# Optimization experiments

Hardware: AMD Instinct MI355X
Metric: run time of the kernel (lower is better)

## Reference

```python
import jax, jax.numpy as jnp
import numpy as np

B, S, HID = 2, 2048, 1024
NH = 16
DK = HID // NH


def setup_inputs() -> dict:
    key0 = jax.random.key(0)
    ks = jax.random.split(key0, 16)
    inp = {
        "query": jax.random.normal(ks[0], (B, S, HID), dtype=jnp.float32),
        "key": jax.random.normal(ks[1], (B, S, HID), dtype=jnp.float32),
        "value": jax.random.normal(ks[2], (B, S, HID), dtype=jnp.float32),
        "bias": jax.random.uniform(ks[3], (B, S), dtype=jnp.float32),
        "mask": jax.random.randint(ks[4], (B, 1, S), 0, 2, dtype=jnp.int32),
        "wq": jax.random.normal(ks[5], (HID, HID), dtype=jnp.float32) * 0.02,
        "bq": jax.random.normal(ks[6], (HID,), dtype=jnp.float32) * 0.02,
        "wk": jax.random.normal(ks[7], (HID, HID), dtype=jnp.float32) * 0.02,
        "bk": jax.random.normal(ks[8], (HID,), dtype=jnp.float32) * 0.02,
        "wv": jax.random.normal(ks[9], (HID, HID), dtype=jnp.float32) * 0.02,
        "bv": jax.random.normal(ks[10], (HID,), dtype=jnp.float32) * 0.02,
        "wo": jax.random.normal(ks[11], (HID, HID), dtype=jnp.float32) * 0.02,
        "bo": jax.random.normal(ks[12], (HID,), dtype=jnp.float32) * 0.02,
    }
    return inp


def reference(query, key, value, bias, mask, wq, bq, wk, bk, wv, bv, wo, bo):
    b, s, hid = query.shape
    # attn_bias_type == 'both': gate K and V with per-token scalar bias
    # (dropout is eval-mode identity): x + p[..., None] * x
    key = key + bias[:, :, None] * key
    value = value + bias[:, :, None] * value

    def proj(x, w, bb):
        # torch Linear: x @ W.T + b, then split heads -> [b, nh, s, dk]
        y = x @ w.T + bb
        return y.reshape(b, s, NH, DK).transpose(0, 2, 1, 3)

    q = proj(query, wq, bq)
    k = proj(key, wk, bk)
    v = proj(value, wv, bv)

    scores = jnp.einsum("bhqd,bhkd->bhqk", q, k) / jnp.sqrt(jnp.asarray(DK, q.dtype))
    m = mask[:, None]  # [b,1,1,s] broadcast over heads and query positions
    scores = jnp.where(m == 0, jnp.asarray(-10000.0, scores.dtype), scores)
    p_attn = jax.nn.softmax(scores, axis=-1)
    x = jnp.einsum("bhqk,bhkd->bhqd", p_attn, v)
    x = x.transpose(0, 2, 1, 3).reshape(b, s, hid)
    return x @ wo.T + bo
```

## Files before the change

### kernel.cpp

```cpp
#include <hip/hip_runtime.h>
#include <stdint.h>

#define NB   2
#define SS   2048
#define HIDN 1024
#define NHEAD 16
#define DKK  64

typedef __attribute__((ext_vector_type(8))) short bf16x8;
typedef __attribute__((ext_vector_type(4))) float f32x4;

__device__ __forceinline__ uint16_t f2bf(float f) {
    uint32_t u = __float_as_uint(f);
    u += 0x7FFF + ((u >> 16) & 1);
    return (uint16_t)(u >> 16);
}
__device__ __forceinline__ uint32_t pk2(float f0, float f1) {
    uint32_t u0 = __float_as_uint(f0);
    uint32_t u1 = __float_as_uint(f1);
    u0 += 0x7FFF + ((u0 >> 16) & 1);
    u1 += 0x7FFF + ((u1 >> 16) & 1);
    return (u0 >> 16) | (u1 & 0xFFFF0000u);
}
__device__ __forceinline__ uint32_t cvtpk(float lo, float hi) {
    uint32_t r;
    asm("v_cvt_pk_bf16_f32 %0, %1, %2" : "=v"(r) : "v"(lo), "v"(hi));
    return r;
}
__device__ __forceinline__ float exp2_fast(float x) {
    float r;
    asm("v_exp_f32 %0, %1" : "=v"(r) : "v"(x));
    return r;
}
__device__ __forceinline__ uint4 pack8(const float* __restrict__ s, float sc) {
    float4 a = *(const float4*)s;
    float4 b = *(const float4*)(s + 4);
    uint4 r;
    r.x = pk2(sc * a.x, sc * a.y);
    r.y = pk2(sc * a.z, sc * a.w);
    r.z = pk2(sc * b.x, sc * b.y);
    r.w = pk2(sc * b.z, sc * b.w);
    return r;
}
__device__ __forceinline__ void gl_lds16(const uint16_t* g, uint16_t* l) {
    __builtin_amdgcn_global_load_lds((const __attribute__((address_space(1))) void*)g,
                                     (__attribute__((address_space(3))) void*)l,
                                     16, 0, 0);
}

__global__ __launch_bounds__(256, 4)
void cvt_all(const float* __restrict__ q, const float* __restrict__ k,
             const float* __restrict__ v, const float* __restrict__ bias,
             const float* __restrict__ w0, const float* __restrict__ w1,
             const float* __restrict__ w2, const float* __restrict__ w3,
             uint16_t* __restrict__ q16, uint16_t* __restrict__ k16,
             uint16_t* __restrict__ v16, uint16_t* __restrict__ w16o)
{
    int i = blockIdx.x * 256 + threadIdx.x;
    if (i < 524288) {
        size_t e = (size_t)i * 8;
        float sc = 1.0f + bias[i >> 7];
        *(uint4*)(q16 + e) = pack8(q + e, 1.0f);
        *(uint4*)(k16 + e) = pack8(k + e, sc);
        *(uint4*)(v16 + e) = pack8(v + e, sc);
    } else {
        int j = i - 524288;
        const float* src = (j < 131072) ? w0 : (j < 262144) ? w1
                         : (j < 393216) ? w2 : w3;
        size_t e = (size_t)(j & 131071) * 8;
        *(uint4*)(w16o + (size_t)(j >> 17) * 1048576 + e) = pack8(src + e, 1.0f);
    }
}

__device__ __forceinline__ void gemm_core(const uint16_t* __restrict__ A,
                                          const uint16_t* __restrict__ W,
                                          uint16_t* __restrict__ As0,
                                          uint16_t* __restrict__ As1,
                                          uint16_t* __restrict__ Bs0,
                                          uint16_t* __restrict__ Bs1,
                                          int m0, int n0,
                                          f32x4 acc[4][2])
{
    const int t    = threadIdx.x;
    const int w    = t >> 6;
    const int lane = t & 63;
    const int q    = lane >> 4;
    const int lr   = lane & 15;
    const int wr   = (w >> 1) * 64;
    const int wc   = (w & 1) * 32;
    const int srow = lane >> 3;
    const int sg   = (lane & 7) ^ srow;

#pragma unroll
    for (int c = 0; c < 4; ++c) {
        int r = w * 32 + c * 8;
        gl_lds16(A + (size_t)(m0 + r + srow) * HIDN + sg * 8, As0 + r * 64);
    }
#pragma unroll
    for (int c = 0; c < 2; ++c) {
        int r = w * 16 + c * 8;
        gl_lds16(W + (size_t)(n0 + r + srow) * HIDN + sg * 8, Bs0 + r * 64);
    }

    for (int it = 0; it < 16; ++it) {
        uint16_t* Asc = (it & 1) ? As1 : As0;
        uint16_t* Bsc = (it & 1) ? Bs1 : Bs0;
        uint16_t* Asn = (it & 1) ? As0 : As1;
        uint16_t* Bsn = (it & 1) ? Bs0 : Bs1;
        __syncthreads();
        if (it + 1 < 16) {
            int k0 = (it + 1) * 64;
#pragma unroll
            for (int c = 0; c < 4; ++c) {
                int r = w * 32 + c * 8;
                gl_lds16(A + (size_t)(m0 + r + srow) * HIDN + k0 + sg * 8,
                         Asn + r * 64);
            }
#pragma unroll
            for (int c = 0; c < 2; ++c) {
                int r = w * 16 + c * 8;
                gl_lds16(W + (size_t)(n0 + r + srow) * HIDN + k0 + sg * 8,
                         Bsn + r * 64);
            }
        }
        bf16x8 af[2][4], bfr[2][2];
#pragma unroll
        for (int s = 0; s < 2; ++s) {
#pragma unroll
            for (int i = 0; i < 4; ++i)
                af[s][i] = *(const bf16x8*)&Asc[(wr + i * 16 + lr) * 64 +
                                                (((s * 4 + q) ^ (lr & 7)) * 8)];
#pragma unroll
            for (int j = 0; j < 2; ++j)
                bfr[s][j] = *(const bf16x8*)&Bsc[(wc + j * 16 + lr) * 64 +
                                                 (((s * 4 + q) ^ (lr & 7)) * 8)];
        }
#pragma unroll
        for (int s = 0; s < 2; ++s)
#pragma unroll
            for (int i = 0; i < 4; ++i)
#pragma unroll
                for (int j = 0; j < 2; ++j)
                    acc[i][j] = __builtin_amdgcn_mfma_f32_16x16x32_bf16(
                        af[s][i], bfr[s][j], acc[i][j], 0, 0, 0);
    }
}

__global__ __launch_bounds__(256, 3)
void gemm_qkv(const uint16_t* __restrict__ Qin, const uint16_t* __restrict__ Kin,
              const uint16_t* __restrict__ Vin, const uint16_t* __restrict__ W16,
              const float* __restrict__ bq, const float* __restrict__ bk,
              const float* __restrict__ bv,
              uint16_t* __restrict__ Qb, uint16_t* __restrict__ Kb,
              uint16_t* __restrict__ Vtb)
{
    __shared__ __align__(16) uint16_t As[2][128 * 64];
    __shared__ __align__(16) uint16_t Bs[2][64 * 64];

    const int z = blockIdx.z;
    const uint16_t* A    = (z == 0) ? Qin : (z == 1) ? Kin : Vin;
    const uint16_t* W    = W16 + (size_t)z * 1048576;
    const float*    bias = (z == 0) ? bq : (z == 1) ? bk : bv;
    const float     osc  = (z == 0) ? 0.125f * 1.44269504f : 1.0f;

    const int t    = threadIdx.x;
    const int w    = t >> 6;
    const int lane = t & 63;
    const int q    = lane >> 4;
    const int lr   = lane & 15;
    const int wr   = (w >> 1) * 64;
    const int wc   = (w & 1) * 32;
    const int m0   = blockIdx.y * 128;
    const int n0   = blockIdx.x * 64;

    f32x4 acc[4][2] = {};
    gemm_core(A, W, As[0], As[1], Bs[0], Bs[1], m0, n0, acc);

    if (z < 2) {
        uint16_t* o = (z == 0) ? Qb : Kb;
#pragma unroll
        for (int i = 0; i < 4; ++i)
#pragma unroll
            for (int j = 0; j < 2; ++j) {
                int gn = n0 + wc + j * 16 + lr;
                float bvx = bias[gn];
#pragma unroll
                for (int r = 0; r < 4; ++r) {
                    int row = m0 + wr + i * 16 + q * 4 + r;
                    int b = row >> 11, s = row & 2047;
                    size_t dst = (size_t)b * (NHEAD * SS * DKK)
                               + (size_t)(gn >> 6) * (SS * DKK)
                               + (size_t)s * DKK + (gn & 63);
                    o[dst] = f2bf((acc[i][j][r] + bvx) * osc);
                }
            }
    } else {
        __syncthreads();
        uint16_t* Tr = (uint16_t*)As;
#pragma unroll
        for (int i = 0; i < 4; ++i)
#pragma unroll
            for (int j = 0; j < 2; ++j) {
                int d = wc + j * 16 + lr;
                float bvx = bias[n0 + d];
#pragma unroll
                for (int r = 0; r < 4; ++r) {
                    int sl = wr + i * 16 + q * 4 + r;
                    Tr[d * 136 + sl] = f2bf(acc[i][j][r] + bvx);
                }
            }
        __syncthreads();
        int b = m0 >> 11, h = n0 >> 6;
#pragma unroll
        for (int p = 0; p < 4; ++p) {
            int idx = p * 256 + t;
            int d   = idx >> 4;
            int sc8 = (idx & 15) * 8;
            size_t dst = ((size_t)(b * NHEAD + h) * DKK + d) * SS
                       + (m0 & 2047) + sc8;
            *(uint4*)&Vtb[dst] = *(const uint4*)&Tr[d * 136 + sc8];
        }
    }
}

__global__ __launch_bounds__(256, 3)
void gemm_out(const uint16_t* __restrict__ Xb, const uint16_t* __restrict__ W,
              const float* __restrict__ bias, float* __restrict__ out)
{
    __shared__ __align__(16) uint16_t As[2][128 * 64];
    __shared__ __align__(16) uint16_t Bs[2][64 * 64];

    const int t    = threadIdx.x;
    const int w    = t >> 6;
    const int lane = t & 63;
    const int q    = lane >> 4;
    const int lr   = lane & 15;
    const int wr   = (w >> 1) * 64;
    const int wc   = (w & 1) * 32;
    const int m0   = blockIdx.y * 128;
    const int n0   = blockIdx.x * 64;

    f32x4 acc[4][2] = {};
    gemm_core(Xb, W, As[0], As[1], Bs[0], Bs[1], m0, n0, acc);

#pragma unroll
    for (int i = 0; i < 4; ++i)
#pragma unroll
        for (int j = 0; j < 2; ++j) {
            int gn = n0 + wc + j * 16 + lr;
            float bvx = bias[gn];
#pragma unroll
            for (int r = 0; r < 4; ++r) {
                int row = m0 + wr + i * 16 + q * 4 + r;
                out[(size_t)row * HIDN + gn] = acc[i][j][r] + bvx;
            }
        }
}

__global__ __launch_bounds__(512, 4)
void flash_attn(const uint16_t* __restrict__ Qg, const uint16_t* __restrict__ Kg,
                const uint16_t* __restrict__ Vtg, const int* __restrict__ mask,
                uint16_t* __restrict__ X)
{
    __shared__ __align__(16) uint16_t QP[128 * 72];
    __shared__ __align__(16) uint16_t Ks[64 * 72];
    __shared__ __align__(16) uint16_t Vs[64 * 72];
    __shared__ __align__(16) float Amf[SS];

    const int t    = threadIdx.x;
    const int w    = t >> 6;
    const int lane = t & 63;
    const int q    = lane >> 4;
    const int lr   = lane & 15;
    const int bh   = blockIdx.y;
    const int b    = bh >> 4;
    const int h    = bh & 15;
    const int q0   = blockIdx.x * 128;
    const size_t head = (size_t)bh * SS * DKK;

#pragma unroll
    for (int p = 0; p < 2; ++p) {
        int idx = p * 512 + t;
        int row = idx >> 3;
        int col = (idx & 7) * 8;
        *(uint4*)&QP[row * 72 + col] =
            *(const uint4*)(Qg + head + (size_t)(q0 + row) * DKK + col);
    }
#pragma unroll
    for (int p = 0; p < 4; ++p) {
        int i = p * 512 + t;
        Amf[i] = (mask[b * SS + i] == 0) ? -14426.95f : 0.0f;
    }

    const int srow = t >> 3;
    const int scol = (t & 7) * 8;
    uint4 kreg = *(const uint4*)(Kg + head + (size_t)srow * DKK + scol);
    uint4 vreg = *(const uint4*)(Vtg + head + (size_t)srow * SS + scol);

    __syncthreads();

    bf16x8 qf[2];
#pragma unroll
    for (int s = 0; s < 2; ++s)
        qf[s] = *(const bf16x8*)&QP[(w * 16 + lr) * 72 + s * 32 + q * 8];

    float mst = -1e30f, lst = 0.0f;
    f32x4 oacc[4] = {};

    for (int kv0 = 0; kv0 < SS; kv0 += 64) {
        *(uint4*)&Ks[srow * 72 + scol] = kreg;
        *(uint4*)&Vs[srow * 72 + scol] = vreg;
        __syncthreads();

        if (kv0 + 64 < SS) {
            kreg = *(const uint4*)(Kg + head + (size_t)(kv0 + 64 + srow) * DKK + scol);
            vreg = *(const uint4*)(Vtg + head + (size_t)srow * SS + kv0 + 64 + scol);
        }

        f32x4 st[4];
#pragma unroll
        for (int ni = 0; ni < 4; ++ni) {
            bf16x8 kf0 = *(const bf16x8*)&Ks[(ni * 16 + lr) * 72 + 0  + q * 8];
            bf16x8 kf1 = *(const bf16x8*)&Ks[(ni * 16 + lr) * 72 + 32 + q * 8];
            f32x4 z = {0.0f, 0.0f, 0.0f, 0.0f};
            z = __builtin_amdgcn_mfma_f32_16x16x32_bf16(kf0, qf[0], z, 0, 0, 0);
            z = __builtin_amdgcn_mfma_f32_16x16x32_bf16(kf1, qf[1], z, 0, 0, 0);
            st[ni] = z;
        }

        float rmax = -1e30f;
#pragma unroll
        for (int ni = 0; ni < 4; ++ni) {
            float4 am = *(const float4*)&Amf[kv0 + ni * 16 + q * 4];
            st[ni][0] += am.x; st[ni][1] += am.y;
            st[ni][2] += am.z; st[ni][3] += am.w;
#pragma unroll
            for (int r = 0; r < 4; ++r) rmax = fmaxf(rmax, st[ni][r]);
        }
        rmax = fmaxf(rmax, __shfl_xor(rmax, 16));
        rmax = fmaxf(rmax, __shfl_xor(rmax, 32));

        if (__any(rmax > mst + 11.5f)) {
            float mnew  = fmaxf(mst, rmax);
            float alpha = exp2_fast(mst - mnew);
            mst = mnew;
            lst *= alpha;
#pragma unroll
            for (int dj = 0; dj < 4; ++dj) {
                oacc[dj][0] *= alpha; oacc[dj][1] *= alpha;
                oacc[dj][2] *= alpha; oacc[dj][3] *= alpha;
            }
        }

        float rsum = 0.0f;
#pragma unroll
        for (int ni = 0; ni < 4; ++ni) {
            float p0 = exp2_fast(st[ni][0] - mst);
            float p1 = exp2_fast(st[ni][1] - mst);
            float p2 = exp2_fast(st[ni][2] - mst);
            float p3 = exp2_fast(st[ni][3] - mst);
            rsum += (p0 + p1) + (p2 + p3);
            uint2 pw = make_uint2(cvtpk(p0, p1), cvtpk(p2, p3));
            *(uint2*)&QP[(w * 16 + lr) * 72 + ni * 16 + q * 4] = pw;
        }
        rsum += __shfl_xor(rsum, 16);
        rsum += __shfl_xor(rsum, 32);
        lst += rsum;

#pragma unroll
        for (int ks = 0; ks < 2; ++ks) {
            bf16x8 pfB = *(const bf16x8*)&QP[(w * 16 + lr) * 72 + ks * 32 + q * 8];
#pragma unroll
            for (int dj = 0; dj < 4; ++dj) {
                bf16x8 vfA = *(const bf16x8*)&Vs[(dj * 16 + lr) * 72 + ks * 32 + q * 8];
                oacc[dj] = __builtin_amdgcn_mfma_f32_16x16x32_bf16(vfA, pfB, oacc[dj], 0, 0, 0);
            }
        }
        __syncthreads();
    }

    {
        float inv = 1.0f / lst;
        int s = q0 + w * 16 + lr;
        uint16_t* xp = X + (size_t)(b * SS + s) * HIDN + h * DKK;
#pragma unroll
        for (int dj = 0; dj < 4; ++dj) {
            uint2 pw = make_uint2(cvtpk(oacc[dj][0] * inv, oacc[dj][1] * inv),
                                  cvtpk(oacc[dj][2] * inv, oacc[dj][3] * inv));
            *(uint2*)(xp + dj * 16 + q * 4) = pw;
        }
    }
}

extern "C" void kernel_launch(void* const* d_in, const int* in_sizes, int n_in,
                              void* d_out, int out_size, void* d_ws, size_t ws_size,
                              hipStream_t stream) {
    const float* query = (const float*)d_in[0];
    const float* key   = (const float*)d_in[1];
    const float* value = (const float*)d_in[2];
    const float* bias  = (const float*)d_in[3];
    const int*   mask  = (const int*)d_in[4];
    const float* wq = (const float*)d_in[5];
    const float* bq = (const float*)d_in[6];
    const float* wk = (const float*)d_in[7];
    const float* bk = (const float*)d_in[8];
    const float* wv = (const float*)d_in[9];
    const float* bv = (const float*)d_in[10];
    const float* wo = (const float*)d_in[11];
    const float* bo = (const float*)d_in[12];

    const size_t TEN = (size_t)NB * SS * HIDN;
    uint16_t* Qin = (uint16_t*)d_ws;
    uint16_t* Kin = Qin + TEN;
    uint16_t* Vin = Kin + TEN;
    uint16_t* W16 = Vin + TEN;
    uint16_t* Qb  = W16 + 4 * 1048576;
    uint16_t* Kb  = Qb + TEN;
    uint16_t* Vtb = Kb + TEN;
    uint16_t* Xb  = Qin;

    cvt_all<<<4096, 256, 0, stream>>>(query, key, value, bias,
                                      wq, wk, wv, wo, Qin, Kin, Vin, W16);
    gemm_qkv<<<dim3(16, 32, 3), 256, 0, stream>>>(Qin, Kin, Vin, W16,
                                                  bq, bk, bv, Qb, Kb, Vtb);
    flash_attn<<<dim3(SS / 128, NB * NHEAD), 512, 0, stream>>>(Qb, Kb, Vtb, mask, Xb);
    gemm_out<<<dim3(16, 32), 256, 0, stream>>>(Xb, W16 + 3 * 1048576, bo, (float*)d_out);
}
```

Measured before the change: 250.2 us.

## Shrink flash-attention blocks to 64 queries with 4 waves and MFMA priority hints

Halves the query tile per block from 128 to 64 rows and runs 4 waves instead of 8, which doubles the grid so more blocks can spread across CUs. Q fragments are now loaded straight from global memory into registers instead of going through shared memory, and the P buffer shrinks to match. Each thread stages two K/V chunks per step. s_setprio raises wave priority around the MFMA sections. The cost is that every K/V tile is loaded and mask-expanded twice as often across the whole grid.

```diff
diff --git a/kernel.cpp b/kernel.cpp
--- a/kernel.cpp
+++ b/kernel.cpp
@@ -257,12 +257,12 @@
         }
 }
 
-__global__ __launch_bounds__(512, 4)
+__global__ __launch_bounds__(256, 4)
 void flash_attn(const uint16_t* __restrict__ Qg, const uint16_t* __restrict__ Kg,
                 const uint16_t* __restrict__ Vtg, const int* __restrict__ mask,
                 uint16_t* __restrict__ X)
 {
-    __shared__ __align__(16) uint16_t QP[128 * 72];
+    __shared__ __align__(16) uint16_t Ps[64 * 72];
     __shared__ __align__(16) uint16_t Ks[64 * 72];
     __shared__ __align__(16) uint16_t Vs[64 * 72];
     __shared__ __align__(16) float Amf[SS];
@@ -275,49 +275,58 @@
     const int bh   = blockIdx.y;
     const int b    = bh >> 4;
     const int h    = bh & 15;
-    const int q0   = blockIdx.x * 128;
+    const int q0   = blockIdx.x * 64;
     const size_t head = (size_t)bh * SS * DKK;
 
-#pragma unroll
-    for (int p = 0; p < 2; ++p) {
-        int idx = p * 512 + t;
-        int row = idx >> 3;
-        int col = (idx & 7) * 8;
-        *(uint4*)&QP[row * 72 + col] =
-            *(const uint4*)(Qg + head + (size_t)(q0 + row) * DKK + col);
-    }
-#pragma unroll
-    for (int p = 0; p < 4; ++p) {
-        int i = p * 512 + t;
+    bf16x8 qf[2];
+#pragma unroll
+    for (int s = 0; s < 2; ++s)
+        qf[s] = *(const bf16x8*)(Qg + head + (size_t)(q0 + w * 16 + lr) * DKK
+                                 + s * 32 + q * 8);
+
+    uint4 kreg[2], vreg[2];
+#pragma unroll
+    for (int c = 0; c < 2; ++c) {
+        int g = c * 256 + t;
+        int row = g >> 3, col = (g & 7) * 8;
+        kreg[c] = *(const uint4*)(Kg + head + (size_t)row * DKK + col);
+        vreg[c] = *(const uint4*)(Vtg + head + (size_t)row * SS + col);
+    }
+
+#pragma unroll
+    for (int p = 0; p < 8; ++p) {
+        int i = p * 256 + t;
         Amf[i] = (mask[b * SS + i] == 0) ? -14426.95f : 0.0f;
     }
-
-    const int srow = t >> 3;
-    const int scol = (t & 7) * 8;
-    uint4 kreg = *(const uint4*)(Kg + head + (size_t)srow * DKK + scol);
-    uint4 vreg = *(const uint4*)(Vtg + head + (size_t)srow * SS + scol);
-
     __syncthreads();
-
-    bf16x8 qf[2];
-#pragma unroll
-    for (int s = 0; s < 2; ++s)
-        qf[s] = *(const bf16x8*)&QP[(w * 16 + lr) * 72 + s * 32 + q * 8];
 
     float mst = -1e30f, lst = 0.0f;
     f32x4 oacc[4] = {};
 
     for (int kv0 = 0; kv0 < SS; kv0 += 64) {
-        *(uint4*)&Ks[srow * 72 + scol] = kreg;
-        *(uint4*)&Vs[srow * 72 + scol] = vreg;
+#pragma unroll
+        for (int c = 0; c < 2; ++c) {
+            int g = c * 256 + t;
+            int row = g >> 3, col = (g & 7) * 8;
+            *(uint4*)&Ks[row * 72 + col] = kreg[c];
+            *(uint4*)&Vs[row * 72 + col] = vreg[c];
+        }
         __syncthreads();
 
         if (kv0 + 64 < SS) {
-            kreg = *(const uint4*)(Kg + head + (size_t)(kv0 + 64 + srow) * DKK + scol);
-            vreg = *(const uint4*)(Vtg + head + (size_t)srow * SS + kv0 + 64 + scol);
+#pragma unroll
+            for (int c = 0; c < 2; ++c) {
+                int g = c * 256 + t;
+                int row = g >> 3, col = (g & 7) * 8;
+                kreg[c] = *(const uint4*)(Kg + head +
+                          (size_t)(kv0 + 64 + row) * DKK + col);
+                vreg[c] = *(const uint4*)(Vtg + head +
+                          (size_t)row * SS + kv0 + 64 + col);
+            }
         }
 
         f32x4 st[4];
+        __builtin_amdgcn_s_setprio(1);
 #pragma unroll
         for (int ni = 0; ni < 4; ++ni) {
             bf16x8 kf0 = *(const bf16x8*)&Ks[(ni * 16 + lr) * 72 + 0  + q * 8];
@@ -327,6 +336,7 @@
             z = __builtin_amdgcn_mfma_f32_16x16x32_bf16(kf1, qf[1], z, 0, 0, 0);
             st[ni] = z;
         }
+        __builtin_amdgcn_s_setprio(0);
 
         float rmax = -1e30f;
 #pragma unroll
@@ -361,21 +371,23 @@
             float p3 = exp2_fast(st[ni][3] - mst);
             rsum += (p0 + p1) + (p2 + p3);
             uint2 pw = make_uint2(cvtpk(p0, p1), cvtpk(p2, p3));
-            *(uint2*)&QP[(w * 16 + lr) * 72 + ni * 16 + q * 4] = pw;
+            *(uint2*)&Ps[(w * 16 + lr) * 72 + ni * 16 + q * 4] = pw;
         }
         rsum += __shfl_xor(rsum, 16);
         rsum += __shfl_xor(rsum, 32);
         lst += rsum;
 
+        __builtin_amdgcn_s_setprio(1);
 #pragma unroll
         for (int ks = 0; ks < 2; ++ks) {
-            bf16x8 pfB = *(const bf16x8*)&QP[(w * 16 + lr) * 72 + ks * 32 + q * 8];
+            bf16x8 pfB = *(const bf16x8*)&Ps[(w * 16 + lr) * 72 + ks * 32 + q * 8];
 #pragma unroll
             for (int dj = 0; dj < 4; ++dj) {
                 bf16x8 vfA = *(const bf16x8*)&Vs[(dj * 16 + lr) * 72 + ks * 32 + q * 8];
                 oacc[dj] = __builtin_amdgcn_mfma_f32_16x16x32_bf16(vfA, pfB, oacc[dj], 0, 0, 0);
             }
         }
+        __builtin_amdgcn_s_setprio(0);
         __syncthreads();
     }
 
@@ -423,6 +435,6 @@
                                       wq, wk, wv, wo, Qin, Kin, Vin, W16);
     gemm_qkv<<<dim3(16, 32, 3), 256, 0, stream>>>(Qin, Kin, Vin, W16,
                                                   bq, bk, bv, Qb, Kb, Vtb);
-    flash_attn<<<dim3(SS / 128, NB * NHEAD), 512, 0, stream>>>(Qb, Kb, Vtb, mask, Xb);
+    flash_attn<<<dim3(SS / 64, NB * NHEAD), 256, 0, stream>>>(Qb, Kb, Vtb, mask, Xb);
     gemm_out<<<dim3(16, 32), 256, 0, stream>>>(Xb, W16 + 3 * 1048576, bo, (float*)d_out);
 }
```

Measured after the change: 323.1 us. +29.1%, slower.

## Enlarge GEMM tiles to 128x128 and drop LDS double buffering

Applied to the files above, without the earlier changes.

The QKV and output projection GEMMs move from 128x64 to 128x128 block tiles, with each wave computing a 64x64 sub-tile, which halves the grid and doubles operand reuse per LDS load. The LDS double buffer is replaced by a single buffer that loads, syncs, computes and syncs again, so global loads no longer overlap MFMA work within a block. The V-transpose epilogue now writes two heads per block through LDS in two passes. This trades latency hiding and occupancy (more accumulator registers, fewer blocks) for less redundant global and LDS traffic.

```diff
diff --git a/kernel.cpp b/kernel.cpp
--- a/kernel.cpp
+++ b/kernel.cpp
@@ -74,12 +74,10 @@
 
 __device__ __forceinline__ void gemm_core(const uint16_t* __restrict__ A,
                                           const uint16_t* __restrict__ W,
-                                          uint16_t* __restrict__ As0,
-                                          uint16_t* __restrict__ As1,
-                                          uint16_t* __restrict__ Bs0,
-                                          uint16_t* __restrict__ Bs1,
+                                          uint16_t* __restrict__ As,
+                                          uint16_t* __restrict__ Bs,
                                           int m0, int n0,
-                                          f32x4 acc[4][2])
+                                          f32x4 acc[4][4])
 {
     const int t    = threadIdx.x;
     const int w    = t >> 6;
@@ -87,62 +85,43 @@
     const int q    = lane >> 4;
     const int lr   = lane & 15;
     const int wr   = (w >> 1) * 64;
-    const int wc   = (w & 1) * 32;
+    const int wc   = (w & 1) * 64;
     const int srow = lane >> 3;
     const int sg   = (lane & 7) ^ srow;
 
-#pragma unroll
-    for (int c = 0; c < 4; ++c) {
-        int r = w * 32 + c * 8;
-        gl_lds16(A + (size_t)(m0 + r + srow) * HIDN + sg * 8, As0 + r * 64);
-    }
-#pragma unroll
-    for (int c = 0; c < 2; ++c) {
-        int r = w * 16 + c * 8;
-        gl_lds16(W + (size_t)(n0 + r + srow) * HIDN + sg * 8, Bs0 + r * 64);
-    }
-
     for (int it = 0; it < 16; ++it) {
-        uint16_t* Asc = (it & 1) ? As1 : As0;
-        uint16_t* Bsc = (it & 1) ? Bs1 : Bs0;
-        uint16_t* Asn = (it & 1) ? As0 : As1;
-        uint16_t* Bsn = (it & 1) ? Bs0 : Bs1;
+        const int k0 = it * 64;
+#pragma unroll
+        for (int c = 0; c < 4; ++c) {
+            int r = w * 32 + c * 8;
+            gl_lds16(A + (size_t)(m0 + r + srow) * HIDN + k0 + sg * 8,
+                     As + r * 64);
+            gl_lds16(W + (size_t)(n0 + r + srow) * HIDN + k0 + sg * 8,
+                     Bs + r * 64);
+        }
         __syncthreads();
-        if (it + 1 < 16) {
-            int k0 = (it + 1) * 64;
-#pragma unroll
-            for (int c = 0; c < 4; ++c) {
-                int r = w * 32 + c * 8;
-                gl_lds16(A + (size_t)(m0 + r + srow) * HIDN + k0 + sg * 8,
-                         Asn + r * 64);
-            }
-#pragma unroll
-            for (int c = 0; c < 2; ++c) {
-                int r = w * 16 + c * 8;
-                gl_lds16(W + (size_t)(n0 + r + srow) * HIDN + k0 + sg * 8,
-                         Bsn + r * 64);
-            }
-        }
-        bf16x8 af[2][4], bfr[2][2];
+
+        bf16x8 af[2][4], bfr[2][4];
 #pragma unroll
         for (int s = 0; s < 2; ++s) {
 #pragma unroll
             for (int i = 0; i < 4; ++i)
-                af[s][i] = *(const bf16x8*)&Asc[(wr + i * 16 + lr) * 64 +
+                af[s][i] = *(const bf16x8*)&As[(wr + i * 16 + lr) * 64 +
+                                               (((s * 4 + q) ^ (lr & 7)) * 8)];
+#pragma unroll
+            for (int j = 0; j < 4; ++j)
+                bfr[s][j] = *(const bf16x8*)&Bs[(wc + j * 16 + lr) * 64 +
                                                 (((s * 4 + q) ^ (lr & 7)) * 8)];
-#pragma unroll
-            for (int j = 0; j < 2; ++j)
-                bfr[s][j] = *(const bf16x8*)&Bsc[(wc + j * 16 + lr) * 64 +
-                                                 (((s * 4 + q) ^ (lr & 7)) * 8)];
         }
 #pragma unroll
         for (int s = 0; s < 2; ++s)
 #pragma unroll
             for (int i = 0; i < 4; ++i)
 #pragma unroll
-                for (int j = 0; j < 2; ++j)
+                for (int j = 0; j < 4; ++j)
                     acc[i][j] = __builtin_amdgcn_mfma_f32_16x16x32_bf16(
                         af[s][i], bfr[s][j], acc[i][j], 0, 0, 0);
+        __syncthreads();
     }
 }
 
@@ -154,8 +133,9 @@
               uint16_t* __restrict__ Qb, uint16_t* __restrict__ Kb,
               uint16_t* __restrict__ Vtb)
 {
-    __shared__ __align__(16) uint16_t As[2][128 * 64];
-    __shared__ __align__(16) uint16_t Bs[2][64 * 64];
+    __shared__ __align__(16) uint16_t Sh[2 * 128 * 64];
+    uint16_t* As = Sh;
+    uint16_t* Bs = Sh + 128 * 64;
 
     const int z = blockIdx.z;
     const uint16_t* A    = (z == 0) ? Qin : (z == 1) ? Kin : Vin;
@@ -169,19 +149,19 @@
     const int q    = lane >> 4;
     const int lr   = lane & 15;
     const int wr   = (w >> 1) * 64;
-    const int wc   = (w & 1) * 32;
+    const int wc   = (w & 1) * 64;
     const int m0   = blockIdx.y * 128;
-    const int n0   = blockIdx.x * 64;
-
-    f32x4 acc[4][2] = {};
-    gemm_core(A, W, As[0], As[1], Bs[0], Bs[1], m0, n0, acc);
+    const int n0   = blockIdx.x * 128;
+
+    f32x4 acc[4][4] = {};
+    gemm_core(A, W, As, Bs, m0, n0, acc);
 
     if (z < 2) {
         uint16_t* o = (z == 0) ? Qb : Kb;
 #pragma unroll
         for (int i = 0; i < 4; ++i)
 #pragma unroll
-            for (int j = 0; j < 2; ++j) {
+            for (int j = 0; j < 4; ++j) {
                 int gn = n0 + wc + j * 16 + lr;
                 float bvx = bias[gn];
 #pragma unroll
@@ -195,30 +175,37 @@
                 }
             }
     } else {
-        __syncthreads();
-        uint16_t* Tr = (uint16_t*)As;
-#pragma unroll
-        for (int i = 0; i < 4; ++i)
-#pragma unroll
-            for (int j = 0; j < 2; ++j) {
-                int d = wc + j * 16 + lr;
-                float bvx = bias[n0 + d];
-#pragma unroll
-                for (int r = 0; r < 4; ++r) {
-                    int sl = wr + i * 16 + q * 4 + r;
-                    Tr[d * 136 + sl] = f2bf(acc[i][j][r] + bvx);
+        uint16_t* Tr = Sh;
+        int b = m0 >> 11;
+#pragma unroll
+        for (int hh = 0; hh < 2; ++hh) {
+            if ((w & 1) == hh) {
+#pragma unroll
+                for (int j = 0; j < 4; ++j) {
+                    int dl = j * 16 + lr;
+                    float bvx = bias[n0 + hh * 64 + dl];
+#pragma unroll
+                    for (int r = 0; r < 4; ++r) {
+                        int sl = wr + (q * 4 + r);
+                        Tr[dl * 136 + sl +  0] = f2bf(acc[0][j][r] + bvx);
+                        Tr[dl * 136 + sl + 16] = f2bf(acc[1][j][r] + bvx);
+                        Tr[dl * 136 + sl + 32] = f2bf(acc[2][j][r] + bvx);
+                        Tr[dl * 136 + sl + 48] = f2bf(acc[3][j][r] + bvx);
+                    }
                 }
             }
-        __syncthreads();
-        int b = m0 >> 11, h = n0 >> 6;
-#pragma unroll
-        for (int p = 0; p < 4; ++p) {
-            int idx = p * 256 + t;
-            int d   = idx >> 4;
-            int sc8 = (idx & 15) * 8;
-            size_t dst = ((size_t)(b * NHEAD + h) * DKK + d) * SS
-                       + (m0 & 2047) + sc8;
-            *(uint4*)&Vtb[dst] = *(const uint4*)&Tr[d * 136 + sc8];
+            __syncthreads();
+            int hgl = (n0 >> 6) + hh;
+#pragma unroll
+            for (int p = 0; p < 4; ++p) {
+                int idx = p * 256 + t;
+                int d   = idx >> 4;
+                int sc8 = (idx & 15) * 8;
+                size_t dst = ((size_t)(b * NHEAD + hgl) * DKK + d) * SS
+                           + (m0 & 2047) + sc8;
+                *(uint4*)&Vtb[dst] = *(const uint4*)&Tr[d * 136 + sc8];
+            }
+            __syncthreads();
         }
     }
 }
@@ -227,8 +214,9 @@
 void gemm_out(const uint16_t* __restrict__ Xb, const uint16_t* __restrict__ W,
               const float* __restrict__ bias, float* __restrict__ out)
 {
-    __shared__ __align__(16) uint16_t As[2][128 * 64];
-    __shared__ __align__(16) uint16_t Bs[2][64 * 64];
+    __shared__ __align__(16) uint16_t Sh[2 * 128 * 64];
+    uint16_t* As = Sh;
+    uint16_t* Bs = Sh + 128 * 64;
 
     const int t    = threadIdx.x;
     const int w    = t >> 6;
@@ -236,17 +224,17 @@
     const int q    = lane >> 4;
     const int lr   = lane & 15;
     const int wr   = (w >> 1) * 64;
-    const int wc   = (w & 1) * 32;
+    const int wc   = (w & 1) * 64;
     const int m0   = blockIdx.y * 128;
-    const int n0   = blockIdx.x * 64;
-
-    f32x4 acc[4][2] = {};
-    gemm_core(Xb, W, As[0], As[1], Bs[0], Bs[1], m0, n0, acc);
+    const int n0   = blockIdx.x * 128;
+
+    f32x4 acc[4][4] = {};
+    gemm_core(Xb, W, As, Bs, m0, n0, acc);
 
 #pragma unroll
     for (int i = 0; i < 4; ++i)
 #pragma unroll
-        for (int j = 0; j < 2; ++j) {
+        for (int j = 0; j < 4; ++j) {
             int gn = n0 + wc + j * 16 + lr;
             float bvx = bias[gn];
 #pragma unroll
@@ -421,8 +409,8 @@
 
     cvt_all<<<4096, 256, 0, stream>>>(query, key, value, bias,
                                       wq, wk, wv, wo, Qin, Kin, Vin, W16);
-    gemm_qkv<<<dim3(16, 32, 3), 256, 0, stream>>>(Qin, Kin, Vin, W16,
-                                                  bq, bk, bv, Qb, Kb, Vtb);
+    gemm_qkv<<<dim3(8, 32, 3), 256, 0, stream>>>(Qin, Kin, Vin, W16,
+                                                 bq, bk, bv, Qb, Kb, Vtb);
     flash_attn<<<dim3(SS / 128, NB * NHEAD), 512, 0, stream>>>(Qb, Kb, Vtb, mask, Xb);
-    gemm_out<<<dim3(16, 32), 256, 0, stream>>>(Xb, W16 + 3 * 1048576, bo, (float*)d_out);
-}
+    gemm_out<<<dim3(8, 32), 256, 0, stream>>>(Xb, W16 + 3 * 1048576, bo, (float*)d_out);
+}
```

Measured after the change: 242.5 us. -3.1%, faster.
